# Kernel optimization log

Measured on AMD Instinct MI355X. Metric: run time of the kernel, lower is better.

Reference implementation:

```python
import jax, jax.numpy as jnp
import numpy as np

H = 768
NH = 12
DH = H // NH  # 64


def setup_inputs() -> dict:
    key = jax.random.key(0)
    ks = jax.random.split(key, 20)
    s = 1.0 / np.sqrt(H)
    def lin(k, din, dout):
        kw, kb = jax.random.split(k)
        W = jax.random.uniform(kw, (din, dout), jnp.float32, -s, s)
        b = jax.random.uniform(kb, (dout,), jnp.float32, -s, s)
        return W, b
    Wq, bq = lin(ks[0], H, H)
    Wk, bk = lin(ks[1], H, H)
    Wv, bv = lin(ks[2], H, H)
    Wt, bt = lin(ks[3], H, H)
    Wi, bi = lin(ks[4], H, H)
    W1, b1 = lin(ks[5], H, H)
    W2, b2 = lin(ks[6], H, 1)
    text = jax.random.normal(ks[7], (8, 64, H), jnp.float32)
    image = jax.random.normal(ks[8], (8, 197, H), jnp.float32)
    return dict(text=text, image=image, Wq=Wq, bq=bq, Wk=Wk, bk=bk, Wv=Wv, bv=bv,
                Wt=Wt, bt=bt, Wi=Wi, bi=bi, W1=W1, b1=b1, W2=W2, b2=b2)


def reference(text, image, Wq, bq, Wk, bk, Wv, bv, Wt, bt, Wi, bi, W1, b1, W2, b2):
    bsz, t_len, _ = text.shape
    i_len = image.shape[1]
    # relevance gate MLP on broadcast product
    text_emb = text @ Wt + bt          # [b, t, H]
    image_emb = image @ Wi + bi        # [b, i, H]
    rel = text_emb[:, :, None, :] * image_emb[:, None, :, :]  # [b, t, i, H]
    rel = jax.nn.relu(rel @ W1 + b1)
    gate = jax.nn.sigmoid(rel @ W2 + b2)  # [b, t, i, 1]
    gate = gate.reshape(bsz, 1, t_len, i_len)
    # cross-attention
    def heads(x, L):
        return x.reshape(bsz, L, NH, DH).transpose(0, 2, 1, 3)  # [b, h, L, dh]
    q = heads(text @ Wq + bq, t_len)
    k = heads(image @ Wk + bk, i_len)
    v = heads(image @ Wv + bv, i_len)
    scores = jnp.einsum('bhtd,bhid->bhti', q, k) / np.sqrt(DH)
    probs = jax.nn.softmax(scores, axis=-1) * gate   # [b, h, t, i]
    ctx = jnp.einsum('bhti,bhid->bhtd', probs, v)    # [b, h, t, dh]
    return ctx.transpose(0, 2, 1, 3).reshape(bsz, t_len, H)
```

## Files before the change

kernel.cpp:

```cpp
#include <hip/hip_runtime.h>
#include <stdint.h>

#define HD 768
#define NHEADS 12
#define DHEAD 64
#define BATCH 8
#define TLEN 64
#define ILEN 197
#define NPAIRS 100864
#define MTILES 394

typedef __attribute__((ext_vector_type(8))) short short8;
typedef __attribute__((ext_vector_type(4))) float f32x4;

__device__ __forceinline__ short f2bf(float x) {
    union { float f; uint32_t u; } v; v.f = x;
    uint32_t r = v.u + 0x7FFFu + ((v.u >> 16) & 1u);
    return (short)(r >> 16);
}
__device__ __forceinline__ float bf2f(short s) {
    union { uint32_t u; float f; } v; v.u = ((uint32_t)(unsigned short)s) << 16;
    return v.f;
}
__device__ __forceinline__ uint32_t cvtpk(float lo, float hi) {
    uint32_t r;
    asm("v_cvt_pk_bf16_f32 %0, %1, %2" : "=v"(r) : "v"(lo), "v"(hi));
    return r;
}
__device__ __forceinline__ void gll16(const void* g, void* l) {
    __builtin_amdgcn_global_load_lds(
        (const __attribute__((address_space(1))) unsigned int*)g,
        (__attribute__((address_space(3))) unsigned int*)l, 16, 0, 0);
}

__global__ __launch_bounds__(256) void prep_weights(
    const float* __restrict__ Wq, const float* __restrict__ Wk,
    const float* __restrict__ Wv, const float* __restrict__ Wt,
    const float* __restrict__ Wi, const float* __restrict__ W1,
    short* __restrict__ W5s, short* __restrict__ W1Bs)
{
    __shared__ float tile[64][65];
    int bx = blockIdx.x;
    int tid = threadIdx.x;
    if (bx >= 720) {
        int idx = bx - 720;
        int pn = idx / 12, kt = idx - pn * 12;
        int c = tid;
        int j = pn * 256 + c;
        char* dst = (char*)W1Bs + (size_t)idx * 32768 + c * 128;
        int swz = (c & 7) << 4;
#pragma unroll
        for (int kg = 0; kg < 8; ++kg) {
            short8 o;
#pragma unroll
            for (int e = 0; e < 8; ++e)
                o[e] = f2bf(W1[(size_t)(kt * 64 + kg * 8 + e) * HD + j]);
            *(short8*)(dst + ((kg * 16) ^ swz)) = o;
        }
        return;
    }
    int seg = bx / 144, ti = bx - seg * 144;
    const float* src = (seg == 0) ? Wt : (seg == 1) ? Wq : (seg == 2) ? Wi
                     : (seg == 3) ? Wk : Wv;
    int kt = ti / 12, ntile = ti - kt * 12;
#pragma unroll
    for (int pass = 0; pass < 16; ++pass) {
        int idx = pass * 256 + tid;
        int kk = idx >> 6, nn = idx & 63;
        tile[kk][nn] = src[(size_t)(kt * 64 + kk) * HD + ntile * 64 + nn];
    }
    __syncthreads();
    size_t base = ((size_t)(seg * 12 + ntile) * 12 + kt) * 8192;
#pragma unroll
    for (int pass = 0; pass < 16; ++pass) {
        int idx = pass * 256 + tid;
        int col = idx >> 6, kloc = idx & 63;
        float x = tile[kloc][col];
        short h = f2bf(x);
        short lw = f2bf(x - bf2f(h));
        int sidx = (col * 64 + kloc) ^ ((col & 7) << 3);
        W5s[base + sidx] = h;
        W5s[base + 4096 + sidx] = lw;
    }
}

__global__ __launch_bounds__(256, 1) void proj_kernel(
    const float* __restrict__ X, int M,
    const short* __restrict__ W5s, int segbase,
    const float* __restrict__ bias0, const float* __restrict__ bias1,
    const float* __restrict__ bias2,
    float* __restrict__ out0, float* __restrict__ out1, float* __restrict__ out2)
{
    __shared__ __align__(16) short Bs[2][8192];
    int tid = threadIdx.x;
    int l = tid & 63, w = tid >> 6;
    int lo = l & 15, grp = l >> 4;
    int y = blockIdx.y;
    int segl = y / 12, ntile = y - segl * 12;
    int seg = segbase + segl;
    const char* wsrc = (const char*)W5s + (size_t)((seg * 12 + ntile) * 12) * 16384;
    {
        const char* s = wsrc + w * 4096 + l * 16;
        char* d = (char*)&Bs[0][0] + w * 4096;
        gll16(s, d); gll16(s + 1024, d + 1024);
        gll16(s + 2048, d + 2048); gll16(s + 3072, d + 3072);
    }
    int arow = blockIdx.x * 64 + w * 16 + lo;
    bool aok = arow < M;
    const float* xrow = X + (size_t)(aok ? arow : 0) * HD;
    short8 ah[24], al[24];
#pragma unroll
    for (int kc = 0; kc < 24; ++kc) {
        int kb = kc * 32 + grp * 8;
        float4 xa = {0.f, 0.f, 0.f, 0.f}, xb = {0.f, 0.f, 0.f, 0.f};
        if (aok) { xa = *(const float4*)(xrow + kb); xb = *(const float4*)(xrow + kb + 4); }
        float xs[8] = {xa.x, xa.y, xa.z, xa.w, xb.x, xb.y, xb.z, xb.w};
#pragma unroll
        for (int e = 0; e < 8; ++e) {
            short hh = f2bf(xs[e]);
            ah[kc][e] = hh;
            al[kc][e] = f2bf(xs[e] - bf2f(hh));
        }
    }
    __syncthreads();

    f32x4 acc[4];
    f32x4 z4 = {0.f, 0.f, 0.f, 0.f};
#pragma unroll
    for (int js = 0; js < 4; ++js) acc[js] = z4;

#pragma unroll
    for (int kk = 0; kk < 12; ++kk) {
        const short* buf = &Bs[kk & 1][0];
        if (kk < 11) {
            const char* s = wsrc + (size_t)(kk + 1) * 16384 + w * 4096 + l * 16;
            char* d = (char*)&Bs[(kk + 1) & 1][0] + w * 4096;
            gll16(s, d); gll16(s + 1024, d + 1024);
            gll16(s + 2048, d + 2048); gll16(s + 3072, d + 3072);
            asm volatile("s_waitcnt vmcnt(4)" ::: "memory");
        } else {
            asm volatile("s_waitcnt vmcnt(0)" ::: "memory");
        }
        __builtin_amdgcn_s_barrier();
        asm volatile("" ::: "memory");
#pragma unroll
        for (int js = 0; js < 4; ++js) {
            int col = js * 16 + lo;
            int base = col * 64;
            int sw = (col & 7) << 3;
#pragma unroll
            for (int kcl = 0; kcl < 2; ++kcl) {
                int idx = (base + kcl * 32 + grp * 8) ^ sw;
                short8 bh = *(const short8*)&buf[idx];
                short8 bl = *(const short8*)&buf[4096 + idx];
                int kc = kk * 2 + kcl;
                acc[js] = __builtin_amdgcn_mfma_f32_16x16x32_bf16(ah[kc], bh, acc[js], 0, 0, 0);
                acc[js] = __builtin_amdgcn_mfma_f32_16x16x32_bf16(ah[kc], bl, acc[js], 0, 0, 0);
                acc[js] = __builtin_amdgcn_mfma_f32_16x16x32_bf16(al[kc], bh, acc[js], 0, 0, 0);
            }
        }
        asm volatile("s_waitcnt lgkmcnt(0)" ::: "memory");
        __builtin_amdgcn_s_barrier();
        asm volatile("" ::: "memory");
    }
    const float* bp = (segl == 0) ? bias0 : (segl == 1) ? bias1 : bias2;
    float* op = (segl == 0) ? out0 : (segl == 1) ? out1 : out2;
#pragma unroll
    for (int js = 0; js < 4; ++js) {
        int cc = ntile * 64 + js * 16 + lo;
        float bvv = bp[cc];
#pragma unroll
        for (int r = 0; r < 4; ++r) {
            int orow = blockIdx.x * 64 + w * 16 + grp * 4 + r;
            if (orow < M) op[(size_t)orow * HD + cc] = acc[js][r] + bvv;
        }
    }
}

__global__ __launch_bounds__(512, 2) void gate_gemm(
    const float* __restrict__ te, const float* __restrict__ ie,
    const short* __restrict__ W1Bs, const float* __restrict__ b1,
    const float* __restrict__ W2, float* __restrict__ plg)
{
    __shared__ __align__(16) char lds[131072];
    int tid = threadIdx.x;
    int lane = tid & 63, wid = tid >> 6;
    int lo = lane & 15, grp = lane >> 4;
    int wr = wid >> 2, wc = wid & 3;
    int bx0 = blockIdx.x;
    int nwg = gridDim.x;
    int qq = nwg >> 3, rr8 = nwg & 7;
    int xcd = bx0 & 7;
    int logical = (xcd < rr8 ? xcd * (qq + 1) : rr8 * (qq + 1) + (xcd - rr8) * qq)
                + (bx0 >> 3);
    int m_l = logical / 3, pn = logical - m_l * 3;

    const char* Bg = (const char*)W1Bs + (size_t)pn * 12 * 32768;

    int crow = wid * 32 + (lane >> 1);
    int ckh  = lane & 1;
    int cp = m_l * 256 + crow;
    int cb = cp / 12608; int crr = cp - cb * 12608;
    int ct_ = crr / 197; int ci = crr - ct_ * 197;
    const float* ctp = te + (size_t)(cb * 64 + ct_) * HD + ckh * 32;
    const float* cip = ie + (size_t)(cb * 197 + ci) * HD + ckh * 32;
    int cawz = (crow & 7) << 4;
    int ckg0 = ckh * 4;

    auto constructA = [&](int t, int par) {
        const float* tpk = ctp + (size_t)t * 64;
        const float* ipk = cip + (size_t)t * 64;
        char* ab = lds + par * 32768 + crow * 128;
#pragma unroll
        for (int g = 0; g < 4; ++g) {
            float4 ta = *(const float4*)(tpk + g * 8);
            float4 tb = *(const float4*)(tpk + g * 8 + 4);
            float4 xa = *(const float4*)(ipk + g * 8);
            float4 xb = *(const float4*)(ipk + g * 8 + 4);
            uint32_t w0 = cvtpk(xa.x * ta.x, xa.y * ta.y);
            uint32_t w1 = cvtpk(xa.z * ta.z, xa.w * ta.w);
            uint32_t w2 = cvtpk(xb.x * tb.x, xb.y * tb.y);
            uint32_t w3 = cvtpk(xb.z * tb.z, xb.w * tb.w);
            uint4 o = {w0, w1, w2, w3};
            *(uint4*)(ab + (((ckg0 + g) * 16) ^ cawz)) = o;
        }
    };

    constructA(0, 0);
    {
        const char* s = Bg + tid * 16;
        char* d = lds + 65536 + tid * 16;
        gll16(s, d); gll16(s + 8192, d + 8192);
        gll16(s + 16384, d + 16384); gll16(s + 24576, d + 24576);
    }
    asm volatile("s_waitcnt vmcnt(0) lgkmcnt(0)" ::: "memory");
    __builtin_amdgcn_s_barrier();
    asm volatile("" ::: "memory");

    f32x4 acc[8][4];
    f32x4 z4 = {0.f, 0.f, 0.f, 0.f};
#pragma unroll
    for (int rt = 0; rt < 8; ++rt)
#pragma unroll
        for (int ct = 0; ct < 4; ++ct) acc[rt][ct] = z4;
    int swz = (lo & 7) << 4;

    for (int kt = 0; kt < 12; ++kt) {
        int par = kt & 1, npar = par ^ 1;
        int aoff = par * 32768;
        int boff = 65536 + par * 32768;
        bool more = kt < 11;

        if (more) constructA(kt + 1, npar);
        if (more) {
            const char* s = Bg + (size_t)(kt + 1) * 32768 + tid * 16;
            char* d = lds + 65536 + npar * 32768 + tid * 16;
            gll16(s, d); gll16(s + 8192, d + 8192);
            gll16(s + 16384, d + 16384); gll16(s + 24576, d + 24576);
        }

        short8 bfr[4][2];
#pragma unroll
        for (int ct = 0; ct < 4; ++ct) {
            int c = wc * 64 + ct * 16 + lo;
#pragma unroll
            for (int ks = 0; ks < 2; ++ks)
                bfr[ct][ks] = *(const short8*)(lds + boff + c * 128 + ((ks * 64 + grp * 16) ^ swz));
        }
#pragma unroll
        for (int q = 0; q < 4; ++q) {
            short8 af[2][2];
#pragma unroll
            for (int i2 = 0; i2 < 2; ++i2) {
                int r = wr * 128 + (2 * q + i2) * 16 + lo;
#pragma unroll
                for (int ks = 0; ks < 2; ++ks)
                    af[i2][ks] = *(const short8*)(lds + aoff + r * 128 + ((ks * 64 + grp * 16) ^ swz));
            }
            __builtin_amdgcn_s_setprio(1);
#pragma unroll
            for (int i2 = 0; i2 < 2; ++i2)
#pragma unroll
                for (int ct = 0; ct < 4; ++ct)
#pragma unroll
                    for (int ks = 0; ks < 2; ++ks)
                        acc[2 * q + i2][ct] = __builtin_amdgcn_mfma_f32_16x16x32_bf16(
                            af[i2][ks], bfr[ct][ks], acc[2 * q + i2][ct], 0, 0, 0);
            __builtin_amdgcn_s_setprio(0);
        }

        asm volatile("s_waitcnt vmcnt(0) lgkmcnt(0)" ::: "memory");
        __builtin_amdgcn_s_barrier();
        asm volatile("" ::: "memory");
    }

    float b1v[4], w2v[4];
#pragma unroll
    for (int ct = 0; ct < 4; ++ct) {
        int j = pn * 256 + wc * 64 + ct * 16 + lo;
        b1v[ct] = b1[j]; w2v[ct] = W2[j];
    }
    float pl[8][4];
#pragma unroll
    for (int rt = 0; rt < 8; ++rt)
#pragma unroll
        for (int r = 0; r < 4; ++r) {
            float s = 0.f;
#pragma unroll
            for (int ct = 0; ct < 4; ++ct)
                s += fmaxf(acc[rt][ct][r] + b1v[ct], 0.f) * w2v[ct];
            pl[rt][r] = s;
        }
#pragma unroll
    for (int msk = 1; msk <= 8; msk <<= 1)
#pragma unroll
        for (int rt = 0; rt < 8; ++rt)
#pragma unroll
            for (int r = 0; r < 4; ++r)
                pl[rt][r] += __shfl_xor(pl[rt][r], msk);

    __syncthreads();
    float* red = (float*)lds;
    if (lo == 0) {
#pragma unroll
        for (int rt = 0; rt < 8; ++rt)
#pragma unroll
            for (int r = 0; r < 4; ++r)
                red[wid * 128 + rt * 16 + grp * 4 + r] = pl[rt][r];
    }
    __syncthreads();
    if (tid < 256) {
        int wr_ = tid >> 7, rl = tid & 127;
        float s = red[(wr_ * 4 + 0) * 128 + rl] + red[(wr_ * 4 + 1) * 128 + rl]
                + red[(wr_ * 4 + 2) * 128 + rl] + red[(wr_ * 4 + 3) * 128 + rl];
        plg[(size_t)pn * NPAIRS + (size_t)m_l * 256 + tid] = s;
    }
}

__global__ __launch_bounds__(256) void gate_fin(
    const float* __restrict__ plg, const float* __restrict__ b2,
    float* __restrict__ gateb)
{
    int idx = blockIdx.x * 256 + threadIdx.x;
    if (idx < NPAIRS) {
        float s = plg[idx] + plg[NPAIRS + idx] + plg[2 * NPAIRS + idx] + b2[0];
        gateb[idx] = 1.f / (1.f + __expf(-s));
    }
}

__global__ __launch_bounds__(256) void attn_kernel(
    const float* __restrict__ q, const float* __restrict__ k,
    const float* __restrict__ v, const float* __restrict__ gate,
    float* __restrict__ out)
{
    __shared__ float k_s[ILEN * 65];
    __shared__ float p_s[4][ILEN][4];
    int bx = blockIdx.x;
    int tq = bx & 3;
    int h = (bx >> 2) % NHEADS;
    int b = bx / (4 * NHEADS);
    int tid = threadIdx.x;
    for (int idx = tid; idx < ILEN * DHEAD; idx += 256) {
        int i = idx >> 6, d = idx & 63;
        k_s[i * 65 + d] = k[(size_t)(b * ILEN + i) * HD + h * DHEAD + d];
    }
    __syncthreads();

    int l = tid & 63, w = tid >> 6;
    int tbase = tq * 16 + w * 4;

    for (int tt = 0; tt < 4; ++tt) {
        int t = tbase + tt;
        float qv = q[(size_t)(b * 64 + t) * HD + h * DHEAD + l];
        float s0 = 0.f, s1 = 0.f, s2 = 0.f, s3 = 0.f;
        int i0 = l, i1 = 64 + l, i2 = 128 + l;
        int i3c = (192 + l < ILEN) ? 192 + l : 0;
        for (int d = 0; d < 64; ++d) {
            float qd = __shfl(qv, d);
            s0 += qd * k_s[i0 * 65 + d];
            s1 += qd * k_s[i1 * 65 + d];
            s2 += qd * k_s[i2 * 65 + d];
            s3 += qd * k_s[i3c * 65 + d];
        }
        float sc[4] = {s0, s1, s2, s3};
        float m = -3.0e38f;
#pragma unroll
        for (int rep = 0; rep < 4; ++rep) {
            int i = rep * 64 + l;
            sc[rep] = (i < ILEN) ? sc[rep] * 0.125f : -3.0e38f;
            m = fmaxf(m, sc[rep]);
        }
        for (int mask = 32; mask >= 1; mask >>= 1) m = fmaxf(m, __shfl_xor(m, mask));
        float sum = 0.f;
#pragma unroll
        for (int rep = 0; rep < 4; ++rep) {
            float e = __expf(sc[rep] - m);
            sc[rep] = e;
            sum += e;
        }
        for (int mask = 32; mask >= 1; mask >>= 1) sum += __shfl_xor(sum, mask);
        float inv = 1.f / sum;
        const float* grow = gate + (size_t)(b * 64 + t) * ILEN;
#pragma unroll
        for (int rep = 0; rep < 4; ++rep) {
            int i = rep * 64 + l;
            if (i < ILEN) p_s[w][i][tt] = sc[rep] * inv * grow[i];
        }
    }

    float ctx[4] = {0.f, 0.f, 0.f, 0.f};
    const float* vbase = v + (size_t)(b * ILEN) * HD + h * DHEAD + l;
#pragma unroll 4
    for (int i = 0; i < ILEN; ++i) {
        float vv = vbase[(size_t)i * HD];
        float4 p4 = *(const float4*)&p_s[w][i][0];
        ctx[0] += p4.x * vv;
        ctx[1] += p4.y * vv;
        ctx[2] += p4.z * vv;
        ctx[3] += p4.w * vv;
    }
#pragma unroll
    for (int tt = 0; tt < 4; ++tt)
        out[(size_t)(b * 64 + tbase + tt) * HD + h * DHEAD + l] = ctx[tt];
}

extern "C" void kernel_launch(void* const* d_in, const int* in_sizes, int n_in,
                              void* d_out, int out_size, void* d_ws, size_t ws_size,
                              hipStream_t stream)
{
    const float* text  = (const float*)d_in[0];
    const float* image = (const float*)d_in[1];
    const float* Wq = (const float*)d_in[2];
    const float* bq = (const float*)d_in[3];
    const float* Wk = (const float*)d_in[4];
    const float* bk = (const float*)d_in[5];
    const float* Wv = (const float*)d_in[6];
    const float* bv = (const float*)d_in[7];
    const float* Wt = (const float*)d_in[8];
    const float* bt = (const float*)d_in[9];
    const float* Wi = (const float*)d_in[10];
    const float* bi = (const float*)d_in[11];
    const float* W1 = (const float*)d_in[12];
    const float* b1 = (const float*)d_in[13];
    const float* W2 = (const float*)d_in[14];
    const float* b2 = (const float*)d_in[15];
    float* out = (float*)d_out;

    char* ws = (char*)d_ws;
    size_t off = 0;
    auto carve = [&](size_t bytes) -> void* {
        void* p = (void*)(ws + off);
        off += (bytes + 255) & ~(size_t)255;
        return p;
    };
    short* W5s  = (short*)carve((size_t)5 * 144 * 8192 * 2);
    short* W1Bs = (short*)carve((size_t)36 * 32768);
    float* te    = (float*)carve((size_t)512 * 768 * 4);
    float* qb    = (float*)carve((size_t)512 * 768 * 4);
    float* ieb   = (float*)carve((size_t)1576 * 768 * 4);
    float* kb    = (float*)carve((size_t)1576 * 768 * 4);
    float* vb    = (float*)carve((size_t)1576 * 768 * 4);
    float* gateb = (float*)carve((size_t)NPAIRS * 4);
    float* plg   = (float*)carve((size_t)3 * NPAIRS * 4);

    hipLaunchKernelGGL(prep_weights, dim3(756), dim3(256), 0, stream,
                       Wq, Wk, Wv, Wt, Wi, W1, W5s, W1Bs);
    hipLaunchKernelGGL(proj_kernel, dim3(8, 24), dim3(256), 0, stream,
                       text, 512, W5s, 0, bt, bq, (const float*)nullptr,
                       te, qb, (float*)nullptr);
    hipLaunchKernelGGL(proj_kernel, dim3(25, 36), dim3(256), 0, stream,
                       image, 1576, W5s, 2, bi, bk, bv,
                       ieb, kb, vb);
    hipLaunchKernelGGL(gate_gemm, dim3(MTILES * 3), dim3(512), 0, stream,
                       te, ieb, W1Bs, b1, W2, plg);
    hipLaunchKernelGGL(gate_fin, dim3((NPAIRS + 255) / 256), dim3(256), 0, stream,
                       plg, b2, gateb);
    hipLaunchKernelGGL(attn_kernel, dim3(BATCH * NHEADS * 4), dim3(256), 0, stream,
                       qb, kb, vb, gateb, out);
}
```

Before: 403.7 us.

## Restructure gate GEMM A-tile construction with LDS-staged text rows and phased MFMA loop

Changes the W1 and A-tile LDS layout to two 64-byte k-halves with a new swizzle, and caches the up-to-three text rows of each block in shared memory so only image rows are read from global memory. The image loads for the next k-tile are issued into registers before the MFMA phases, and the multiply and bf16 pack run afterwards, overlapping global latency with compute. The MFMA loop is split into four phases with barriers between them, and launch bounds drop to one block per SM. The added barriers, the higher register pressure and the lower occupancy may offset the saved loads.

```diff
diff --git a/kernel.cpp b/kernel.cpp
--- a/kernel.cpp
+++ b/kernel.cpp
@@ -47,15 +47,19 @@
         int pn = idx / 12, kt = idx - pn * 12;
         int c = tid;
         int j = pn * 256 + c;
-        char* dst = (char*)W1Bs + (size_t)idx * 32768 + c * 128;
-        int swz = (c & 7) << 4;
-#pragma unroll
-        for (int kg = 0; kg < 8; ++kg) {
-            short8 o;
-#pragma unroll
-            for (int e = 0; e < 8; ++e)
-                o[e] = f2bf(W1[(size_t)(kt * 64 + kg * 8 + e) * HD + j]);
-            *(short8*)(dst + ((kg * 16) ^ swz)) = o;
+        char* chunk = (char*)W1Bs + (size_t)idx * 32768;
+        int f = (c >> 1) & 3;
+#pragma unroll
+        for (int ks = 0; ks < 2; ++ks) {
+            char* dst = chunk + ks * 16384 + c * 64;
+#pragma unroll
+            for (int g = 0; g < 4; ++g) {
+                short8 o;
+#pragma unroll
+                for (int e = 0; e < 8; ++e)
+                    o[e] = f2bf(W1[(size_t)(kt * 64 + ks * 32 + g * 8 + e) * HD + j]);
+                *(short8*)(dst + ((g * 16) ^ (f << 4))) = o;
+            }
         }
         return;
     }
@@ -177,12 +181,14 @@
     }
 }
 
-__global__ __launch_bounds__(512, 2) void gate_gemm(
+__global__ __launch_bounds__(512, 1) void gate_gemm(
     const float* __restrict__ te, const float* __restrict__ ie,
     const short* __restrict__ W1Bs, const float* __restrict__ b1,
     const float* __restrict__ W2, float* __restrict__ plg)
 {
     __shared__ __align__(16) char lds[131072];
+    __shared__ float te_s[3 * HD];
+    __shared__ int ieoff[256];
     int tid = threadIdx.x;
     int lane = tid & 63, wid = tid >> 6;
     int lo = lane & 15, grp = lane >> 4;
@@ -196,37 +202,41 @@
     int m_l = logical / 3, pn = logical - m_l * 3;
 
     const char* Bg = (const char*)W1Bs + (size_t)pn * 12 * 32768;
-
-    int crow = wid * 32 + (lane >> 1);
-    int ckh  = lane & 1;
-    int cp = m_l * 256 + crow;
-    int cb = cp / 12608; int crr = cp - cb * 12608;
-    int ct_ = crr / 197; int ci = crr - ct_ * 197;
-    const float* ctp = te + (size_t)(cb * 64 + ct_) * HD + ckh * 32;
-    const float* cip = ie + (size_t)(cb * 197 + ci) * HD + ckh * 32;
-    int cawz = (crow & 7) << 4;
-    int ckg0 = ckh * 4;
-
-    auto constructA = [&](int t, int par) {
-        const float* tpk = ctp + (size_t)t * 64;
-        const float* ipk = cip + (size_t)t * 64;
-        char* ab = lds + par * 32768 + crow * 128;
-#pragma unroll
-        for (int g = 0; g < 4; ++g) {
-            float4 ta = *(const float4*)(tpk + g * 8);
-            float4 tb = *(const float4*)(tpk + g * 8 + 4);
-            float4 xa = *(const float4*)(ipk + g * 8);
-            float4 xb = *(const float4*)(ipk + g * 8 + 4);
-            uint32_t w0 = cvtpk(xa.x * ta.x, xa.y * ta.y);
-            uint32_t w1 = cvtpk(xa.z * ta.z, xa.w * ta.w);
-            uint32_t w2 = cvtpk(xb.x * tb.x, xb.y * tb.y);
-            uint32_t w3 = cvtpk(xb.z * tb.z, xb.w * tb.w);
-            uint4 o = {w0, w1, w2, w3};
-            *(uint4*)(ab + (((ckg0 + g) * 16) ^ cawz)) = o;
+    int bt0 = (m_l * 256) / 197;
+
+    if (tid < 256) {
+        int p = m_l * 256 + tid;
+        int bt = p / 197;
+        int i = p - bt * 197;
+        int b = bt >> 6;
+        ieoff[tid] = (b * 197 + i) * HD | ((bt - bt0) << 24);
+    }
+    for (int idx = tid; idx < 3 * HD; idx += 512) {
+        int r = idx / HD;
+        int bt = bt0 + r; if (bt > 511) bt = 511;
+        te_s[idx] = te[(size_t)bt * HD + (idx - r * HD)];
+    }
+    __syncthreads();
+
+    auto constructA0 = [&](int t, int par) {
+#pragma unroll
+        for (int u = 0; u < 8; ++u) {
+            int w = u * 512 + tid;
+            int row = w >> 4, f4 = w & 15;
+            int pk = ieoff[row];
+            float4 x = *(const float4*)(ie + (pk & 0xFFFFFF) + t * 64 + f4 * 4);
+            const float* tp = &te_s[(pk >> 24) * HD + t * 64 + f4 * 4];
+            float4 tv = *(const float4*)tp;
+            uint32_t o0 = cvtpk(x.x * tv.x, x.y * tv.y);
+            uint32_t o1 = cvtpk(x.z * tv.z, x.w * tv.w);
+            int ks = f4 >> 3, r7 = f4 & 7, g = r7 >> 1, half = r7 & 1;
+            char* dst = lds + par * 32768 + ks * 16384 + row * 64
+                      + ((g * 16) ^ (((row >> 1) & 3) << 4)) + half * 8;
+            uint2 o = {o0, o1};
+            *(uint2*)dst = o;
         }
     };
-
-    constructA(0, 0);
+    constructA0(0, 0);
     {
         const char* s = Bg + tid * 16;
         char* d = lds + 65536 + tid * 16;
@@ -243,7 +253,6 @@
     for (int rt = 0; rt < 8; ++rt)
 #pragma unroll
         for (int ct = 0; ct < 4; ++ct) acc[rt][ct] = z4;
-    int swz = (lo & 7) << 4;
 
     for (int kt = 0; kt < 12; ++kt) {
         int par = kt & 1, npar = par ^ 1;
@@ -251,45 +260,79 @@
         int boff = 65536 + par * 32768;
         bool more = kt < 11;
 
-        if (more) constructA(kt + 1, npar);
+        float4 xi[8];
         if (more) {
+#pragma unroll
+            for (int u = 0; u < 8; ++u) {
+                int w = u * 512 + tid;
+                int row = w >> 4, f4 = w & 15;
+                int pk = ieoff[row];
+                xi[u] = *(const float4*)(ie + (pk & 0xFFFFFF) + (kt + 1) * 64 + f4 * 4);
+            }
             const char* s = Bg + (size_t)(kt + 1) * 32768 + tid * 16;
             char* d = lds + 65536 + npar * 32768 + tid * 16;
             gll16(s, d); gll16(s + 8192, d + 8192);
             gll16(s + 16384, d + 16384); gll16(s + 24576, d + 24576);
         }
 
-        short8 bfr[4][2];
-#pragma unroll
-        for (int ct = 0; ct < 4; ++ct) {
-            int c = wc * 64 + ct * 16 + lo;
-#pragma unroll
-            for (int ks = 0; ks < 2; ++ks)
-                bfr[ct][ks] = *(const short8*)(lds + boff + c * 128 + ((ks * 64 + grp * 16) ^ swz));
-        }
-#pragma unroll
-        for (int q = 0; q < 4; ++q) {
-            short8 af[2][2];
-#pragma unroll
-            for (int i2 = 0; i2 < 2; ++i2) {
-                int r = wr * 128 + (2 * q + i2) * 16 + lo;
-#pragma unroll
-                for (int ks = 0; ks < 2; ++ks)
-                    af[i2][ks] = *(const short8*)(lds + aoff + r * 128 + ((ks * 64 + grp * 16) ^ swz));
-            }
+        short8 bfr[4], af[4];
+#pragma unroll
+        for (int ph = 0; ph < 4; ++ph) {
+            int ksp = ph >> 1;
+            int rh  = ph & 1;
+            if (rh == 0) {
+#pragma unroll
+                for (int ct = 0; ct < 4; ++ct) {
+                    int c = wc * 64 + ct * 16 + lo;
+                    bfr[ct] = *(const short8*)(lds + boff + ksp * 16384 + c * 64
+                                + ((grp * 16) ^ (((c >> 1) & 3) << 4)));
+                }
+            }
+#pragma unroll
+            for (int j = 0; j < 4; ++j) {
+                int r = wr * 128 + (rh * 4 + j) * 16 + lo;
+                af[j] = *(const short8*)(lds + aoff + ksp * 16384 + r * 64
+                            + ((grp * 16) ^ (((r >> 1) & 3) << 4)));
+            }
+            __builtin_amdgcn_s_barrier();
+            asm volatile("s_waitcnt lgkmcnt(0)" ::: "memory");
+            __builtin_amdgcn_sched_barrier(0);
             __builtin_amdgcn_s_setprio(1);
 #pragma unroll
-            for (int i2 = 0; i2 < 2; ++i2)
+            for (int j = 0; j < 4; ++j)
 #pragma unroll
                 for (int ct = 0; ct < 4; ++ct)
-#pragma unroll
-                    for (int ks = 0; ks < 2; ++ks)
-                        acc[2 * q + i2][ct] = __builtin_amdgcn_mfma_f32_16x16x32_bf16(
-                            af[i2][ks], bfr[ct][ks], acc[2 * q + i2][ct], 0, 0, 0);
+                    acc[rh * 4 + j][ct] = __builtin_amdgcn_mfma_f32_16x16x32_bf16(
+                        af[j], bfr[ct], acc[rh * 4 + j][ct], 0, 0, 0);
             __builtin_amdgcn_s_setprio(0);
-        }
-
-        asm volatile("s_waitcnt vmcnt(0) lgkmcnt(0)" ::: "memory");
+            if (ph < 3) {
+                __builtin_amdgcn_s_barrier();
+                asm volatile("" ::: "memory");
+            }
+        }
+
+        if (more) {
+            asm volatile("s_waitcnt vmcnt(0)" ::: "memory");
+#pragma unroll
+            for (int u = 0; u < 8; ++u) {
+                int w = u * 512 + tid;
+                int row = w >> 4, f4 = w & 15;
+                int pk = ieoff[row];
+                const float* tp = &te_s[(pk >> 24) * HD + (kt + 1) * 64 + f4 * 4];
+                float4 tv = *(const float4*)tp;
+                float4 x = xi[u];
+                uint32_t o0 = cvtpk(x.x * tv.x, x.y * tv.y);
+                uint32_t o1 = cvtpk(x.z * tv.z, x.w * tv.w);
+                int ks = f4 >> 3, r7 = f4 & 7, g = r7 >> 1, half = r7 & 1;
+                char* dst = lds + npar * 32768 + ks * 16384 + row * 64
+                          + ((g * 16) ^ (((row >> 1) & 3) << 4)) + half * 8;
+                uint2 o = {o0, o1};
+                *(uint2*)dst = o;
+            }
+        } else {
+            asm volatile("s_waitcnt vmcnt(0)" ::: "memory");
+        }
+        asm volatile("s_waitcnt lgkmcnt(0)" ::: "memory");
         __builtin_amdgcn_s_barrier();
         asm volatile("" ::: "memory");
     }
```

Result: faster. 336.0 us (-16.8%).
